# Kernel tuning notes

Hardware: AMD Instinct MI355X
Metric: run time of the kernel (lower is better)

The kernel has to match this reference:

```python
import jax, jax.numpy as jnp
import numpy as np

N, C, H, W = 8, 256, 31, 31
HIDDEN, OUT = 512, 256


def setup_inputs() -> dict:
    key = jax.random.key(0)
    k0, k1, k2, k3, k4 = jax.random.split(key, 5)
    x = jax.random.normal(k0, (N, C, H, W), dtype=jnp.float32)
    # Linear params (torch nn.Linear layout: [out_features, in_features])
    W1 = jax.random.normal(k1, (HIDDEN, C), dtype=jnp.float32) * (1.0 / np.sqrt(C))
    b1 = jax.random.normal(k2, (HIDDEN,), dtype=jnp.float32) * 0.01
    W2 = jax.random.normal(k3, (OUT, HIDDEN), dtype=jnp.float32) * (1.0 / np.sqrt(HIDDEN))
    b2 = jax.random.normal(k4, (OUT,), dtype=jnp.float32) * 0.01
    return {"x": x, "W1": W1, "b1": b1, "W2": W2, "b2": b2}


def _normalized_adjacency(n, h, w):
    M = n * h * w
    idx = jnp.arange(M)
    blk = idx // (h * w)          # sample id of each node
    pos = idx % (h * w)           # spatial position within sample
    # block-diagonal all-ones per sample
    same_block = (blk[:, None] == blk[None, :]).astype(jnp.float32)
    # identity link between consecutive samples (disjoint from block-diag)
    neighbor = ((jnp.abs(blk[:, None] - blk[None, :]) == 1)
                & (pos[:, None] == pos[None, :])).astype(jnp.float32)
    A = same_block + neighbor + jnp.eye(M, dtype=jnp.float32)
    deg = A.sum(axis=1)
    dinv = jnp.where(deg > 0, deg ** -0.5, 0.0)
    return A * dinv[:, None] * dinv[None, :]  # D^-1/2 A D^-1/2


def reference(x, W1, b1, W2, b2):
    n, c, h, w = x.shape
    weight = _normalized_adjacency(n, h, w)                 # [M, M]
    nodes = x.transpose(0, 2, 3, 1).reshape(-1, c)          # [M, C]
    hid = jax.nn.leaky_relu(weight @ nodes @ W1.T + b1)     # [M, HIDDEN]
    hid = jax.nn.leaky_relu(weight @ hid @ W2.T + b2)       # [M, OUT]
    hid = hid.reshape(n, h, w, -1).transpose(0, 3, 1, 2)    # [N, OUT, H, W]
    return hid.max(axis=0, keepdims=True)                   # [1, OUT, H, W]
```

## Files before the change

### kernel.cpp

```cpp
#include <hip/hip_runtime.h>
#include <math.h>

#define NS   8
#define CC   256
#define PP   961
#define MM   7688
#define MP   7744
#define HID  512
#define OUTC 256

typedef _Float16 h16;
using half4   = __attribute__((ext_vector_type(4))) _Float16;
using half8   = __attribute__((ext_vector_type(8))) _Float16;
using floatx4 = __attribute__((ext_vector_type(4))) float;

#define AS1 __attribute__((address_space(1)))
#define AS3 __attribute__((address_space(3)))

__device__ __forceinline__ float dinv_of(int b) {
    return (b == 0 || b == NS - 1) ? 0.0322245515f : 0.0322078318f;
}

__global__ void prep(const float* __restrict__ W1, const float* __restrict__ W2,
                     h16* __restrict__ w1h, h16* __restrict__ w2h,
                     const float* __restrict__ x, float* __restrict__ S1,
                     float* __restrict__ SY) {
    int blk = blockIdx.x, tid = threadIdx.x;
    if (blk < 256) {
        bool second = blk >= 128;
        const float* src = second ? W2 : W1;
        h16* dst = second ? w2h : w1h;
        int i = ((blk & 127) * 256 + tid) * 4;
        float4 v = *(const float4*)(src + i);
        half4 h = { (h16)v.x, (h16)v.y, (h16)v.z, (h16)v.w };
        *(half4*)(dst + i) = h;
    } else if (blk < 768) {
        int wave = tid >> 6, lane = tid & 63;
        int row = (blk - 256) * 4 + wave;
        const float* src = x + (size_t)row * PP;
        float s = 0.f;
        for (int i = lane; i < PP; i += 64) s += src[i];
        #pragma unroll
        for (int off = 32; off; off >>= 1) s += __shfl_xor(s, off);
        if (lane == 0) S1[row] = s;
    } else {
        int i = (blk - 768) * 256 + tid;
        SY[i] = 0.f;
    }
}

__global__ void build_g1(const float* __restrict__ x, const float* __restrict__ S1,
                         h16* __restrict__ G1) {
    int pt = blockIdx.x, ct = blockIdx.y, b = blockIdx.z;
    int p0 = pt * 32, c0 = ct * 64;
    float db  = dinv_of(b);
    float wm  = (b > 0)      ? db * dinv_of(b - 1) : 0.f;
    float wp  = (b < NS - 1) ? db * dinv_of(b + 1) : 0.f;
    float db2 = db * db;
    __shared__ float t[64][33];
    int j = threadIdx.x & 31, i0 = threadIdx.x >> 5;
    int p = p0 + j;
    bool pv = (p < PP);
    #pragma unroll
    for (int r = 0; r < 8; ++r) {
        int i = i0 + r * 8;
        int c = c0 + i;
        float v = 0.f;
        if (pv) {
            size_t base = ((size_t)b * CC + c) * PP + p;
            float xb = x[base];
            float xm = (b > 0)      ? x[base - (size_t)CC * PP] : 0.f;
            float xp = (b < NS - 1) ? x[base + (size_t)CC * PP] : 0.f;
            v = db2 * (S1[b * CC + c] + xb) + wm * xm + wp * xp;
        }
        t[i][j] = v;
    }
    __syncthreads();
    int chunk = threadIdx.x & 7, prow = threadIdx.x >> 3;
    int pw = p0 + prow;
    if (pw < PP) {
        half8 h;
        #pragma unroll
        for (int q = 0; q < 8; ++q) h[q] = (h16)t[chunk * 8 + q][prow];
        *(half8*)&G1[((size_t)b * PP + pw) * CC + c0 + chunk * 8] = h;
    }
}

template<int KD, bool ACT, bool DO_SUM, typename OutT>
__global__ __launch_bounds__(256) void mfma_gemm(
    const h16* __restrict__ A,
    const h16* __restrict__ B,
    const float* __restrict__ bias,
    OutT* __restrict__ C,
    float* __restrict__ SY,
    int M, int Nc)
{
    __shared__ __align__(16) h16 As[64 * 64];
    __shared__ __align__(16) h16 Bs[64 * 64];
    int tid = threadIdx.x, wave = tid >> 6, lane = tid & 63;
    int m0 = blockIdx.x * 64, n0 = blockIdx.y * 64;
    int sro = lane >> 3;
    int sch = (lane & 7) ^ sro;
    const h16* ga0 = A + (size_t)(m0 + wave * 16 + sro) * KD + sch * 8;
    const h16* gb0 = B + (size_t)(n0 + wave * 16 + sro) * KD + sch * 8;
    h16* la0 = &As[(wave * 16) * 64];
    h16* la1 = &As[(wave * 16 + 8) * 64];
    h16* lb0 = &Bs[(wave * 16) * 64];
    h16* lb1 = &Bs[(wave * 16 + 8) * 64];
    int fr = lane & 15, fq = lane >> 4;
    floatx4 acc[4] = {{0.f,0.f,0.f,0.f},{0.f,0.f,0.f,0.f},{0.f,0.f,0.f,0.f},{0.f,0.f,0.f,0.f}};
    for (int kk = 0; kk < KD; kk += 64) {
        __builtin_amdgcn_global_load_lds((const AS1 void*)(const void*)(ga0 + kk),
                                         (AS3 void*)(void*)la0, 16, 0, 0);
        __builtin_amdgcn_global_load_lds((const AS1 void*)(const void*)(ga0 + 8 * KD + kk),
                                         (AS3 void*)(void*)la1, 16, 0, 0);
        __builtin_amdgcn_global_load_lds((const AS1 void*)(const void*)(gb0 + kk),
                                         (AS3 void*)(void*)lb0, 16, 0, 0);
        __builtin_amdgcn_global_load_lds((const AS1 void*)(const void*)(gb0 + 8 * KD + kk),
                                         (AS3 void*)(void*)lb1, 16, 0, 0);
        __syncthreads();
        #pragma unroll
        for (int ks = 0; ks < 2; ++ks) {
            int slot = (ks * 4 + fq) ^ (fr & 7);
            half8 bf = *(const half8*)&Bs[(wave * 16 + fr) * 64 + slot * 8];
            #pragma unroll
            for (int mb = 0; mb < 4; ++mb) {
                half8 af = *(const half8*)&As[(mb * 16 + fr) * 64 + slot * 8];
                acc[mb] = __builtin_amdgcn_mfma_f32_16x16x32_f16(af, bf, acc[mb], 0, 0, 0);
            }
        }
        __syncthreads();
    }
    int col = n0 + wave * 16 + fr;
    float bv = ACT ? bias[col] : 0.f;
    float s_lo = 0.f, s_hi = 0.f;
    int blo = m0 / 961;
    int mcut = (blo + 1) * 961;
    #pragma unroll
    for (int mb = 0; mb < 4; ++mb) {
        #pragma unroll
        for (int r = 0; r < 4; ++r) {
            int m = m0 + mb * 16 + fq * 4 + r;
            if (m < M) {
                float v = acc[mb][r] + bv;
                if (ACT) v = (v >= 0.f) ? v : 0.01f * v;
                C[(size_t)m * Nc + col] = (OutT)v;
                if (DO_SUM) { if (m < mcut) s_lo += v; else s_hi += v; }
            }
        }
    }
    if (DO_SUM) {
        s_lo += __shfl_xor(s_lo, 16);
        s_lo += __shfl_xor(s_lo, 32);
        s_hi += __shfl_xor(s_hi, 16);
        s_hi += __shfl_xor(s_hi, 32);
        if (fq == 0) {
            atomicAdd(&SY[blo * Nc + col], s_lo);
            int bhi = (m0 + 63) / 961;
            if (bhi != blo && bhi < NS) atomicAdd(&SY[bhi * Nc + col], s_hi);
        }
    }
}

__global__ void final_max(const float* __restrict__ Y, const float* __restrict__ SY,
                          const float* __restrict__ b2, float* __restrict__ out) {
    int pt = blockIdx.x, ot = blockIdx.y;
    int p0 = pt * 32, o0 = ot * 32;
    __shared__ float t[32][33];
    int i = threadIdx.x & 31, j0 = threadIdx.x >> 5;
    int o = o0 + i;
    float bias = b2[o];
    #pragma unroll
    for (int r = 0; r < 4; ++r) {
        int j = j0 + r * 8;
        int p = p0 + j;
        float vmax = -INFINITY;
        if (p < PP) {
            float y[NS];
            #pragma unroll
            for (int b = 0; b < NS; ++b)
                y[b] = Y[((size_t)b * PP + p) * OUTC + o];
            #pragma unroll
            for (int b = 0; b < NS; ++b) {
                float db = dinv_of(b);
                float a = db * (SY[b * OUTC + o] + y[b]);
                if (b > 0)      a += dinv_of(b - 1) * y[b - 1];
                if (b < NS - 1) a += dinv_of(b + 1) * y[b + 1];
                float z = db * a + bias;
                z = (z >= 0.f) ? z : 0.01f * z;
                vmax = fmaxf(vmax, z);
            }
        }
        t[j][i] = vmax;
    }
    __syncthreads();
    int jj = threadIdx.x & 31, ii0 = threadIdx.x >> 5;
    #pragma unroll
    for (int r = 0; r < 4; ++r) {
        int ii = ii0 + r * 8;
        int pw = p0 + jj;
        if (pw < PP)
            out[(size_t)(o0 + ii) * PP + pw] = t[jj][ii];
    }
}

extern "C" void kernel_launch(void* const* d_in, const int* in_sizes, int n_in,
                              void* d_out, int out_size, void* d_ws, size_t ws_size,
                              hipStream_t stream) {
    const float* x  = (const float*)d_in[0];
    const float* W1 = (const float*)d_in[1];
    const float* b1 = (const float*)d_in[2];
    const float* W2 = (const float*)d_in[3];
    const float* b2 = (const float*)d_in[4];
    float* out = (float*)d_out;
    float* ws  = (float*)d_ws;

    float* S1  = ws;
    float* SY  = ws + 2048;
    h16*  w1h  = (h16*)(ws + 4096);
    h16*  w2h  = (h16*)(ws + 69632);
    h16*  G1   = (h16*)(ws + 135168);
    h16*  H1   = (h16*)(ws + 1126400);
    float* Y   = ws + 3108864;

    prep<<<776, 256, 0, stream>>>(W1, W2, w1h, w2h, x, S1, SY);
    build_g1<<<dim3(31, 4, NS), 256, 0, stream>>>(x, S1, G1);
    mfma_gemm<CC, true, false, h16><<<dim3(MP / 64, HID / 64), 256, 0, stream>>>(
        G1, w1h, b1, H1, nullptr, MM, HID);
    mfma_gemm<HID, false, true, float><<<dim3(MP / 64, OUTC / 64), 256, 0, stream>>>(
        H1, w2h, nullptr, Y, SY, MM, OUTC);
    final_max<<<dim3(31, 8), 256, 0, stream>>>(Y, SY, b2, out);
}
```

Baseline: 99.87 us.

## Stage GEMM epilogue through LDS for vectorized row stores; widen row-sum blocks

The GEMM epilogue now writes the accumulator tile into padded shared memory that reuses the operand buffers, then each thread stores 16 contiguous elements of a row with vector stores. The old epilogue issued scattered per-element column stores. Separately, the per-(sample,channel) spatial sum in prep now uses one 256-thread block per row with a shared-memory tree reduction instead of one wave per row. This adds an extra barrier and an LDS round trip per tile, and makes the sum reduction heavier in synchronization.

```diff
diff --git a/kernel.cpp b/kernel.cpp
--- a/kernel.cpp
+++ b/kernel.cpp
@@ -34,17 +34,21 @@
         float4 v = *(const float4*)(src + i);
         half4 h = { (h16)v.x, (h16)v.y, (h16)v.z, (h16)v.w };
         *(half4*)(dst + i) = h;
-    } else if (blk < 768) {
-        int wave = tid >> 6, lane = tid & 63;
-        int row = (blk - 256) * 4 + wave;
-        const float* src = x + (size_t)row * PP;
+    } else if (blk < 2304) {
+        int bc = blk - 256;
+        const float* src = x + (size_t)bc * PP;
         float s = 0.f;
-        for (int i = lane; i < PP; i += 64) s += src[i];
-        #pragma unroll
-        for (int off = 32; off; off >>= 1) s += __shfl_xor(s, off);
-        if (lane == 0) S1[row] = s;
+        for (int i = tid; i < PP; i += 256) s += src[i];
+        __shared__ float red[256];
+        red[tid] = s;
+        __syncthreads();
+        for (int off = 128; off > 0; off >>= 1) {
+            if (tid < off) red[tid] += red[tid + off];
+            __syncthreads();
+        }
+        if (tid == 0) S1[bc] = red[0];
     } else {
-        int i = (blk - 768) * 256 + tid;
+        int i = (blk - 2304) * 256 + tid;
         SY[i] = 0.f;
     }
 }
@@ -95,8 +99,12 @@
     float* __restrict__ SY,
     int M, int Nc)
 {
-    __shared__ __align__(16) h16 As[64 * 64];
-    __shared__ __align__(16) h16 Bs[64 * 64];
+    constexpr int EPAD = (sizeof(OutT) == 2) ? 72 : 68;
+    constexpr int EPI_BYTES = 64 * EPAD * (int)sizeof(OutT);
+    constexpr int SMEM_BYTES = EPI_BYTES > 16384 ? EPI_BYTES : 16384;
+    __shared__ __align__(16) unsigned char smem[SMEM_BYTES];
+    h16* As = (h16*)smem;
+    h16* Bs = (h16*)(smem + 8192);
     int tid = threadIdx.x, wave = tid >> 6, lane = tid & 63;
     int m0 = blockIdx.x * 64, n0 = blockIdx.y * 64;
     int sro = lane >> 3;
@@ -132,20 +140,38 @@
         __syncthreads();
     }
     int col = n0 + wave * 16 + fr;
+    int cloc = wave * 16 + fr;
     float bv = ACT ? bias[col] : 0.f;
     float s_lo = 0.f, s_hi = 0.f;
     int blo = m0 / 961;
     int mcut = (blo + 1) * 961;
+    OutT* Ts = (OutT*)smem;
     #pragma unroll
     for (int mb = 0; mb < 4; ++mb) {
         #pragma unroll
         for (int r = 0; r < 4; ++r) {
-            int m = m0 + mb * 16 + fq * 4 + r;
-            if (m < M) {
-                float v = acc[mb][r] + bv;
-                if (ACT) v = (v >= 0.f) ? v : 0.01f * v;
-                C[(size_t)m * Nc + col] = (OutT)v;
-                if (DO_SUM) { if (m < mcut) s_lo += v; else s_hi += v; }
+            int row = mb * 16 + fq * 4 + r;
+            int m = m0 + row;
+            float v = acc[mb][r] + bv;
+            if (ACT) v = (v >= 0.f) ? v : 0.01f * v;
+            Ts[row * EPAD + cloc] = (OutT)v;
+            if (DO_SUM && m < M) { if (m < mcut) s_lo += v; else s_hi += v; }
+        }
+    }
+    __syncthreads();
+    {
+        int row = tid >> 2, seg = tid & 3;
+        int m = m0 + row;
+        if (m < M) {
+            const OutT* src = Ts + row * EPAD + seg * 16;
+            OutT* dst = C + (size_t)m * Nc + n0 + seg * 16;
+            if constexpr (sizeof(OutT) == 2) {
+                *(half8*)(dst)     = *(const half8*)(src);
+                *(half8*)(dst + 8) = *(const half8*)(src + 8);
+            } else {
+                #pragma unroll
+                for (int q = 0; q < 4; ++q)
+                    *(float4*)((float*)dst + q * 4) = *(const float4*)((const float*)src + q * 4);
             }
         }
     }
@@ -223,7 +249,7 @@
     h16*  H1   = (h16*)(ws + 1126400);
     float* Y   = ws + 3108864;
 
-    prep<<<776, 256, 0, stream>>>(W1, W2, w1h, w2h, x, S1, SY);
+    prep<<<2312, 256, 0, stream>>>(W1, W2, w1h, w2h, x, S1, SY);
     build_g1<<<dim3(31, 4, NS), 256, 0, stream>>>(x, S1, G1);
     mfma_gemm<CC, true, false, h16><<<dim3(MP / 64, HID / 64), 256, 0, stream>>>(
         G1, w1h, b1, H1, nullptr, MM, HID);
```

Result: no change. 98.37 us (-1.5%).
